# Performance work log

Measured on AMD Instinct MI355X. Metric: run time of the kernel, lower is better.

## Reference

```python
import jax, jax.numpy as jnp
import numpy as np

L = 4096
PI = 3.141592653589793
# cfg weights (V23Config defaults used here)
W_BOND, W_ANGLE, W_RAMA, W_CLASH = 1.0, 1.0, 0.5, 2.0
W_HBOND, W_ELECTRO, W_SOLVENT, W_ROTAMER = 1.0, 0.5, 0.5, 0.5
W_AENT, W_ASMOOTH = 0.01, 0.01
CA_CA_DIST, ANGLE_TARGET_RAD, CLASH_RADIUS = 3.8, 1.5708, 4.0
MOD_BOND, MOD_ANGLE, MOD_CLASH, MOD_HBOND, MOD_RAMA = 0.1, 0.1, 0.1, 0.1, 0.1

# per-residue tables in AA_VOCAB order 'ACDEFGHIKLMNPQRSTVWYX'
CHARGE_TAB = np.zeros(21, np.float32); CHARGE_TAB[[2, 3]] = -1.0; CHARGE_TAB[[8, 14]] = 1.0; CHARGE_TAB[6] = 0.5
HYDRO_TAB = np.array([1.8, 2.5, -3.5, -3.5, 2.8, -0.4, -3.2, 4.5, -3.9, 3.8, 1.9, -3.5, -1.6, -3.5, -4.5, -0.8, -0.7, 4.2, -0.9, -1.3, 0.0], np.float32)
PHI0_TAB = np.full(21, -60.0, np.float32); PHI0_TAB[5] = -75.0; PHI0_TAB[12] = -65.0
PSI0_TAB = np.full(21, -45.0, np.float32); PSI0_TAB[5] = -60.0; PSI0_TAB[12] = -30.0
WID_TAB = np.full(21, 25.0, np.float32); WID_TAB[5] = 40.0; WID_TAB[12] = 20.0
GLY_ID = 5


def _normalize(x, eps=1e-8):
    return x / jnp.maximum(jnp.linalg.norm(x, axis=-1, keepdims=True), eps)


def _cdist(a, b):
    d2 = jnp.sum(a * a, -1)[:, None] + jnp.sum(b * b, -1)[None, :] - 2.0 * (a @ b.T)
    return jnp.sqrt(jnp.maximum(d2, 0.0))


def _dihedral(p0, p1, p2, p3):
    b0, b1, b2 = p1 - p0, p2 - p1, p3 - p2
    b1n = _normalize(b1)
    v = b0 - jnp.sum(b0 * b1n, -1, keepdims=True) * b1n
    w = b2 - jnp.sum(b2 * b1n, -1, keepdims=True) * b1n
    x = jnp.sum(v * w, -1)
    y = jnp.sum(jnp.cross(b1n, v) * w, -1)
    return jnp.arctan2(y + 1e-8, x + 1e-8)


def _energy(ca, alpha, seq_ids):
    Lr = ca.shape[0]
    charge = jnp.asarray(CHARGE_TAB)[seq_ids]
    hydro = jnp.asarray(HYDRO_TAB)[seq_ids]
    phi0 = jnp.asarray(PHI0_TAB)[seq_ids]
    psi0 = jnp.asarray(PSI0_TAB)[seq_ids]
    width = jnp.asarray(WID_TAB)[seq_ids]
    is_gly = seq_ids == GLY_ID

    # ---- reconstruct backbone N, C, O from the CA trace ----
    vn = _normalize(ca[1:] - ca[:-1])  # [L-1,3]
    Natm = jnp.concatenate([ca[:1] - 1.45 * vn[:1], ca[1:] - 1.45 * vn], 0)
    Catm = jnp.concatenate([ca[:-1] + 1.52 * vn, ca[-1:] + 1.52 * vn[-1:]], 0)
    perp = jnp.cross(Catm - ca, Natm - ca)
    pn = jnp.linalg.norm(perp, axis=-1, keepdims=True)
    perp = jnp.where(pn > 1e-6, perp / jnp.maximum(pn, 1e-30), perp)
    Oatm = jnp.concatenate([(Catm + 1.24 * perp)[:-1], Catm[-1:] + jnp.array([0.0, 1.24, 0.0], ca.dtype)], 0)

    # ---- phi/psi dihedrals in degrees ----
    deg = 180.0 / PI
    phi = jnp.zeros(Lr, ca.dtype).at[1:-1].set(_dihedral(Catm[:-2], Natm[1:-1], ca[1:-1], Catm[1:-1])) * deg
    psi = jnp.zeros(Lr, ca.dtype).at[1:-1].set(_dihedral(Natm[1:-1], ca[1:-1], Catm[1:-1], Natm[2:])) * deg

    # ---- bond ----
    target = CA_CA_DIST * (1.0 + MOD_BOND * (alpha - 1.0))
    tpair = 0.5 * (target[1:] + target[:-1])
    d = jnp.linalg.norm(ca[1:] - ca[:-1], axis=-1)
    e_bond = W_BOND * jnp.mean((d - tpair) ** 2)

    # ---- angle ----
    v1 = _normalize(ca[:-2] - ca[1:-1])
    v2 = _normalize(ca[2:] - ca[1:-1])
    cos_ang = jnp.sum(v1 * v2, -1)
    cos_t = jnp.cos(ANGLE_TARGET_RAD * (1.0 + MOD_ANGLE * (alpha[1:-1] - 1.0)))
    e_angle = W_ANGLE * jnp.mean((cos_ang - cos_t) ** 2)

    # ---- rama ----
    weff = width * (1.0 + MOD_RAMA * (alpha - 1.0))
    dphi = (phi - phi0) / (weff + 1e-8)
    dpsi = (psi - psi0) / (weff + 1e-8)
    rmask = jnp.ones(Lr, bool).at[0].set(False).at[-1].set(False)
    e_rama = W_RAMA * jnp.sum((dphi ** 2 + dpsi ** 2) * rmask) / jnp.maximum(1, jnp.sum(rmask))

    D = _cdist(ca, ca)  # [L,L]

    # ---- clash: NOTE the original torch code's advanced indexing
    # mask[idx[:,None], idx[None,:]] = False broadcasts over the FULL grid,
    # so the mask is entirely False and this term is identically zero.
    # Reproduced faithfully (same math).
    radius = CLASH_RADIUS * (1.0 + MOD_CLASH * (alpha[:, None] - 1.0))
    rpair = 0.5 * (radius + radius.T)
    clash = jax.nn.relu(rpair - D) * jnp.zeros((Lr, Lr), ca.dtype)
    e_clash = W_CLASH * jnp.mean(clash ** 2)

    # ---- electrostatics (screened Coulomb) ----
    De = D + 1e-6
    Ee = charge[:, None] * charge[None, :] * jnp.exp(-0.1 * De) / (80.0 * De)
    Ee = Ee * (1.0 - jnp.eye(Lr, dtype=ca.dtype))
    e_electro = W_ELECTRO * jnp.mean(Ee)

    # ---- hydrogen bonds ----
    Dh = _cdist(Oatm, Natm)
    hmask = (Dh > 2.5) & (Dh < 3.5)
    vec_co = (Oatm - Catm)[:, None, :]          # [L,1,3]
    vec_no = Natm[None, :, :] - Oatm[:, None, :]  # [L,L,3]
    num = jnp.sum(vec_co * vec_no, -1)
    den = jnp.maximum(jnp.linalg.norm(vec_co, axis=-1), 1e-8) * jnp.maximum(jnp.linalg.norm(vec_no, axis=-1), 1e-8)
    align = num / den
    ideal = 2.9 * (1.0 + MOD_HBOND * (alpha[:, None] - 1.0))
    Eh = -align * jnp.exp(-(((Dh - ideal) / 0.3) ** 2))
    e_hbond = W_HBOND * jnp.mean(Eh * hmask)

    # ---- solvent / burial ----
    density = jnp.sum((D < 10.0).astype(ca.dtype), -1)
    burial = 1.0 - jnp.exp(-density / 20.0)
    exposed = jnp.where(hydro > 0, hydro * (1.0 - burial), 0.0)
    buried = jnp.where(hydro <= 0, -hydro * burial, 0.0)
    e_solv = W_SOLVENT * jnp.mean(exposed + buried)

    # ---- rotamer (vectorized over residues; skips G and chain ends) ----
    cb_dir = _normalize(-((Natm - ca) + (Catm - ca)))
    ideal_cb = ca + 1.8 * cb_dir
    Dr = _cdist(ideal_cb, ca) + jnp.eye(Lr, dtype=ca.dtype) * 1e9  # exclude self
    dmin = jnp.min(Dr, -1)
    pos = jnp.arange(Lr)
    inc = (~is_gly) & (pos > 0) & (pos < Lr - 1)
    e_rot = W_ROTAMER * jnp.sum(jax.nn.relu(4.0 - dmin) * inc) / max(1, Lr - 2)

    # ---- alpha regularisation ----
    ent = -jnp.mean(alpha * jnp.log(alpha + 1e-8))
    smooth = jnp.mean((alpha[1:] - alpha[:-1]) ** 2)
    e_alpha = W_AENT * ent + W_ASMOOTH * smooth

    return e_bond + e_angle + e_rama + e_clash + e_hbond + e_electro + e_solv + e_rot + e_alpha


def setup_inputs() -> dict:
    key = jax.random.key(0)
    k1, k2, k3 = jax.random.split(key, 3)
    ca = jax.random.normal(k1, (L, 3), jnp.float32) * 10.0  # spread-out CA trace (Angstrom scale)
    alpha = jax.random.uniform(k2, (L,), jnp.float32, 0.5, 3.0)  # AdaptiveAlphaField range
    seq_ids = jax.random.randint(k3, (L,), 0, 21)
    return {"ca": ca, "alpha": alpha, "seq_ids": seq_ids}


def reference(ca, alpha, seq_ids):
    return _energy(ca, alpha, seq_ids)
```

## Files before the change

### kernel.cpp

```cpp
#include <hip/hip_runtime.h>
#include <math.h>

#define L 4096
#define JC 32
#define NJB (L/JC)
#define NIB 8
#define NBLK (NIB*NJB)

__constant__ float c_charge[21] = {0.f,0.f,-1.f,-1.f,0.f,0.f,0.5f,0.f,1.f,0.f,0.f,0.f,0.f,0.f,1.f,0.f,0.f,0.f,0.f,0.f,0.f};
__constant__ float c_hydro[21]  = {1.8f,2.5f,-3.5f,-3.5f,2.8f,-0.4f,-3.2f,4.5f,-3.9f,3.8f,1.9f,-3.5f,-1.6f,-3.5f,-4.5f,-0.8f,-0.7f,4.2f,-0.9f,-1.3f,0.f};
__constant__ float c_phi0[21]   = {-60.f,-60.f,-60.f,-60.f,-60.f,-75.f,-60.f,-60.f,-60.f,-60.f,-60.f,-60.f,-65.f,-60.f,-60.f,-60.f,-60.f,-60.f,-60.f,-60.f,-60.f};
__constant__ float c_psi0[21]   = {-45.f,-45.f,-45.f,-45.f,-45.f,-60.f,-45.f,-45.f,-45.f,-45.f,-45.f,-45.f,-30.f,-45.f,-45.f,-45.f,-45.f,-45.f,-45.f,-45.f,-45.f};
__constant__ float c_wid[21]    = {25.f,25.f,25.f,25.f,25.f,40.f,25.f,25.f,25.f,25.f,25.f,25.f,20.f,25.f,25.f,25.f,25.f,25.f,25.f,25.f,25.f};

#define WS_PA(ws)   ((float4*)(ws))
#define WS_PB(ws)   ((float4*)((ws)+4*L))
#define WS_PI1(ws)  ((float4*)((ws)+8*L))
#define WS_PI2(ws)  ((float4*)((ws)+12*L))
#define WS_PI3(ws)  ((float4*)((ws)+16*L))
#define WS_DENS(ws) ((ws)+20*L)
#define WS_DMIN(ws) ((unsigned int*)((ws)+21*L))
#define WS_RP(ws)   ((ws)+22*L)
#define WS_BPEL(ws) ((ws)+22*L+320)
#define WS_BPHB(ws) ((ws)+22*L+320+NBLK)

struct f3 { float x, y, z; };
__device__ inline f3 mk(float x, float y, float z){ f3 r{x,y,z}; return r; }
__device__ inline f3 sub3(f3 a, f3 b){ return mk(a.x-b.x, a.y-b.y, a.z-b.z); }
__device__ inline f3 add3(f3 a, f3 b){ return mk(a.x+b.x, a.y+b.y, a.z+b.z); }
__device__ inline f3 scl3(f3 a, float s){ return mk(a.x*s, a.y*s, a.z*s); }
__device__ inline float dot3(f3 a, f3 b){ return a.x*b.x + a.y*b.y + a.z*b.z; }
__device__ inline f3 crs3(f3 a, f3 b){ return mk(a.y*b.z-a.z*b.y, a.z*b.x-a.x*b.z, a.x*b.y-a.y*b.x); }
__device__ inline float nrm3(f3 a){ return sqrtf(dot3(a,a)); }
__device__ inline f3 unit3(f3 a){ float n = fmaxf(nrm3(a), 1e-8f); return mk(a.x/n, a.y/n, a.z/n); }

__device__ inline float dihedral(f3 p0, f3 p1, f3 p2, f3 p3){
  f3 b0 = sub3(p1,p0), b1 = sub3(p2,p1), b2 = sub3(p3,p2);
  f3 b1n = unit3(b1);
  f3 v = sub3(b0, scl3(b1n, dot3(b0,b1n)));
  f3 w = sub3(b2, scl3(b1n, dot3(b2,b1n)));
  float x = dot3(v,w);
  float y = dot3(crs3(b1n,v), w);
  return atan2f(y + 1e-8f, x + 1e-8f);
}

__device__ inline float wave_reduce(float v){
  #pragma unroll
  for (int off = 32; off > 0; off >>= 1) v += __shfl_down(v, off, 64);
  return v;
}

__global__ __launch_bounds__(64) void residue_kernel(const float* __restrict__ ca,
    const float* __restrict__ alpha, const int* __restrict__ seq, float* __restrict__ ws)
{
  int i = blockIdx.x*64 + threadIdx.x;
  f3 c0 = mk(ca[3*i], ca[3*i+1], ca[3*i+2]);
  f3 cm = c0, cp = c0;
  if (i > 0)   cm = mk(ca[3*(i-1)], ca[3*(i-1)+1], ca[3*(i-1)+2]);
  if (i < L-1) cp = mk(ca[3*(i+1)], ca[3*(i+1)+1], ca[3*(i+1)+2]);
  f3 vnm = unit3(sub3(c0, cm));
  f3 vni = unit3(sub3(cp, c0));

  f3 N = (i == 0)  ? sub3(c0, scl3(vni, 1.45f)) : sub3(c0, scl3(vnm, 1.45f));
  f3 C = (i < L-1) ? add3(c0, scl3(vni, 1.52f)) : add3(c0, scl3(vnm, 1.52f));
  f3 perp = crs3(sub3(C,c0), sub3(N,c0));
  float pn = nrm3(perp);
  if (pn > 1e-6f) perp = scl3(perp, 1.f/fmaxf(pn, 1e-30f));
  f3 O = (i < L-1) ? add3(C, scl3(perp, 1.24f)) : mk(C.x, C.y + 1.24f, C.z);

  f3 sum = add3(sub3(N,c0), sub3(C,c0));
  f3 cbdir = unit3(mk(-sum.x, -sum.y, -sum.z));
  f3 cb = add3(c0, scl3(cbdir, 1.8f));

  f3 vco = sub3(O, C);
  float nco = fmaxf(nrm3(vco), 1e-8f);

  int sid = seq[i];
  float al = alpha[i];

  float4 pa; pa.x=c0.x; pa.y=c0.y; pa.z=c0.z; pa.w=c_charge[sid];
  float4 pb; pb.x=N.x; pb.y=N.y; pb.z=N.z; pb.w=0.f;
  float4 p1; p1.x=O.x; p1.y=O.y; p1.z=O.z; p1.w=nco;
  float4 p2; p2.x=vco.x; p2.y=vco.y; p2.z=vco.z; p2.w=2.9f*(1.f + 0.1f*(al - 1.f));
  float4 p3; p3.x=cb.x; p3.y=cb.y; p3.z=cb.z; p3.w=0.f;
  WS_PA(ws)[i]=pa; WS_PB(ws)[i]=pb; WS_PI1(ws)[i]=p1; WS_PI2(ws)[i]=p2; WS_PI3(ws)[i]=p3;
  WS_DENS(ws)[i]=0.f;
  WS_DMIN(ws)[i]=0x7F800000u;

  float bond = 0.f, angle = 0.f, rama = 0.f, smooth = 0.f;
  float ent = al * logf(al + 1e-8f);
  if (i < L-1) {
    float alp = alpha[i+1];
    float d = nrm3(sub3(cp, c0));
    float tp = 0.5f*(3.8f*(1.f+0.1f*(al-1.f)) + 3.8f*(1.f+0.1f*(alp-1.f)));
    bond = (d - tp)*(d - tp);
    smooth = (alp - al)*(alp - al);
  }
  if (i >= 1 && i <= L-2) {
    f3 v1 = unit3(sub3(cm, c0));
    f3 v2 = unit3(sub3(cp, c0));
    float cang = dot3(v1, v2);
    float ct = cosf(1.5708f*(1.f + 0.1f*(al - 1.f)));
    angle = (cang - ct)*(cang - ct);

    f3 Cm1 = add3(cm, scl3(vnm, 1.52f));
    f3 Np1 = sub3(cp, scl3(vni, 1.45f));
    const float deg = 57.29577951308232f;
    float phi = dihedral(Cm1, N, c0, C) * deg;
    float psi = dihedral(N, c0, C, Np1) * deg;
    float weff = c_wid[sid]*(1.f + 0.1f*(al - 1.f)) + 1e-8f;
    float dphi = (phi - c_phi0[sid]) / weff;
    float dpsi = (psi - c_psi0[sid]) / weff;
    rama = dphi*dphi + dpsi*dpsi;
  }
  bond = wave_reduce(bond); angle = wave_reduce(angle); rama = wave_reduce(rama);
  ent  = wave_reduce(ent);  smooth = wave_reduce(smooth);
  if (threadIdx.x == 0) {
    float* RP = WS_RP(ws);
    int b = blockIdx.x;
    RP[0*64+b]=bond; RP[1*64+b]=angle; RP[2*64+b]=rama; RP[3*64+b]=ent; RP[4*64+b]=smooth;
  }
}

__global__ __launch_bounds__(256) void pair_kernel(float* __restrict__ ws)
{
  const float4* __restrict__ PA  = WS_PA(ws);
  const float4* __restrict__ PB  = WS_PB(ws);
  const float4* __restrict__ PI1 = WS_PI1(ws);
  const float4* __restrict__ PI2 = WS_PI2(ws);
  const float4* __restrict__ PI3 = WS_PI3(ws);

  int t = threadIdx.x;
  int i0 = blockIdx.x*512 + t;
  int i1 = i0 + 256;
  int j0 = blockIdx.y*JC;

  __shared__ float4 sA[JC];
  __shared__ float4 sB[JC];
  if (t < JC)           sA[t]     = PA[j0 + t];
  else if (t < 2*JC)    sB[t-JC]  = PB[j0 + t - JC];

  float4 a0 = PA[i0],  a1 = PA[i1];
  float4 o0 = PI1[i0], o1 = PI1[i1];
  float4 w0 = PI2[i0], w1 = PI2[i1];
  float4 g0 = PI3[i0], g1 = PI3[i1];
  float rn0 = __builtin_amdgcn_rcpf(o0.w);
  float rn1 = __builtin_amdgcn_rcpf(o1.w);
  __syncthreads();

  float e_el = 0.f, e_hb = 0.f;
  float dens0 = 0.f, dens1 = 0.f, dm0 = 3.0e38f, dm1 = 3.0e38f;

  #pragma unroll 8
  for (int jj = 0; jj < JC; ++jj) {
    float4 a = sA[jj];
    float4 b = sB[jj];
    int jg = j0 + jj;
    bool self0 = (jg == i0), self1 = (jg == i1);

    float dx0 = a0.x - a.x, dy0 = a0.y - a.y, dz0 = a0.z - a.z;
    float d20 = fmaf(dx0,dx0, fmaf(dy0,dy0, dz0*dz0));
    float dx1 = a1.x - a.x, dy1 = a1.y - a.y, dz1 = a1.z - a.z;
    float d21 = fmaf(dx1,dx1, fmaf(dy1,dy1, dz1*dz1));
    dens0 += (d20 < 100.f) ? 1.f : 0.f;
    dens1 += (d21 < 100.f) ? 1.f : 0.f;

    float rx0 = g0.x - a.x, ry0 = g0.y - a.y, rz0 = g0.z - a.z;
    float r20 = fmaf(rx0,rx0, fmaf(ry0,ry0, rz0*rz0));
    dm0 = fminf(dm0, self0 ? 3.0e38f : r20);
    float rx1 = g1.x - a.x, ry1 = g1.y - a.y, rz1 = g1.z - a.z;
    float r21 = fmaf(rx1,rx1, fmaf(ry1,ry1, rz1*rz1));
    dm1 = fminf(dm1, self1 ? 3.0e38f : r21);

    if (a.w != 0.f) {
      float qq0 = self0 ? 0.f : a0.w * a.w;
      float D0  = sqrtf(d20) + 1e-6f;
      e_el += qq0 * __expf(-0.1f*D0) * __builtin_amdgcn_rcpf(80.f*D0);
      float qq1 = self1 ? 0.f : a1.w * a.w;
      float D1  = sqrtf(d21) + 1e-6f;
      e_el += qq1 * __expf(-0.1f*D1) * __builtin_amdgcn_rcpf(80.f*D1);
    }

    float nx0 = b.x - o0.x, ny0 = b.y - o0.y, nz0 = b.z - o0.z;
    float h20 = fmaf(nx0,nx0, fmaf(ny0,ny0, nz0*nz0));
    if (h20 > 6.25f && h20 < 12.25f) {
      float rs  = __builtin_amdgcn_rsqf(h20);
      float Dh  = h20 * rs;
      float num = fmaf(w0.x,nx0, fmaf(w0.y,ny0, w0.z*nz0));
      float tt  = (Dh - w0.w) * 3.33333333333333f;
      e_hb -= num * (rn0 * rs) * __expf(-tt*tt);
    }
    float nx1 = b.x - o1.x, ny1 = b.y - o1.y, nz1 = b.z - o1.z;
    float h21 = fmaf(nx1,nx1, fmaf(ny1,ny1, nz1*nz1));
    if (h21 > 6.25f && h21 < 12.25f) {
      float rs  = __builtin_amdgcn_rsqf(h21);
      float Dh  = h21 * rs;
      float num = fmaf(w1.x,nx1, fmaf(w1.y,ny1, w1.z*nz1));
      float tt  = (Dh - w1.w) * 3.33333333333333f;
      e_hb -= num * (rn1 * rs) * __expf(-tt*tt);
    }
  }

  e_el = wave_reduce(e_el);
  e_hb = wave_reduce(e_hb);
  __shared__ float sp[8];
  if ((t & 63) == 0) { sp[t>>6] = e_el; sp[4+(t>>6)] = e_hb; }
  __syncthreads();
  if (t == 0) {
    int bidx = blockIdx.y*NIB + blockIdx.x;
    WS_BPEL(ws)[bidx] = sp[0]+sp[1]+sp[2]+sp[3];
    WS_BPHB(ws)[bidx] = sp[4]+sp[5]+sp[6]+sp[7];
  }
  atomicAdd(&WS_DENS(ws)[i0], dens0);
  atomicAdd(&WS_DENS(ws)[i1], dens1);
  atomicMin(&WS_DMIN(ws)[i0], __float_as_uint(dm0));
  atomicMin(&WS_DMIN(ws)[i1], __float_as_uint(dm1));
}

__global__ __launch_bounds__(1024) void final_kernel(const int* __restrict__ seq,
    const float* __restrict__ ws, float* __restrict__ out)
{
  int t = threadIdx.x;
  const float* BPel = WS_BPEL(ws);
  const float* BPhb = WS_BPHB(ws);
  const float* RP = WS_RP(ws);

  float v0=0.f,v1=0.f,v2=0.f,v3=0.f,v4=0.f,v7=0.f,v8=0.f;
  float v5 = BPel[t];
  float v6 = BPhb[t];
  if (t < 64) { v0=RP[t]; v1=RP[64+t]; v2=RP[128+t]; v3=RP[192+t]; v4=RP[256+t]; }

  #pragma unroll
  for (int k = 0; k < 4; ++k) {
    int i = t + k*1024;
    float density = WS_DENS((float*)ws)[i];
    float burial = 1.f - __expf(-density * 0.05f);
    float hy = c_hydro[seq[i]];
    v7 += (hy > 0.f) ? hy*(1.f - burial) : (-hy*burial);
    float dmin = sqrtf(__uint_as_float(((const unsigned int*)(ws+21*L))[i]));
    if (seq[i] != 5 && i > 0 && i < L-1) v8 += fmaxf(4.f - dmin, 0.f);
  }

  v0=wave_reduce(v0); v1=wave_reduce(v1); v2=wave_reduce(v2);
  v3=wave_reduce(v3); v4=wave_reduce(v4); v5=wave_reduce(v5);
  v6=wave_reduce(v6); v7=wave_reduce(v7); v8=wave_reduce(v8);

  __shared__ float red[16*9];
  int w = t >> 6;
  if ((t & 63) == 0) {
    red[w*9+0]=v0; red[w*9+1]=v1; red[w*9+2]=v2; red[w*9+3]=v3; red[w*9+4]=v4;
    red[w*9+5]=v5; red[w*9+6]=v6; red[w*9+7]=v7; red[w*9+8]=v8;
  }
  __syncthreads();
  if (t == 0) {
    float s[9];
    #pragma unroll
    for (int q = 0; q < 9; ++q) s[q] = 0.f;
    for (int ww = 0; ww < 16; ++ww)
      #pragma unroll
      for (int q = 0; q < 9; ++q) s[q] += red[ww*9+q];
    const float Lf = (float)L;
    out[0] = s[0] / (Lf - 1.f)
           + s[1] / (Lf - 2.f)
           + 0.5f * s[2] / (Lf - 2.f)
           + 0.5f * s[5] / (Lf * Lf)
           + s[6] / (Lf * Lf)
           + 0.5f * s[7] / Lf
           + 0.5f * s[8] / (Lf - 2.f)
           + 0.01f * (-s[3] / Lf)
           + 0.01f * s[4] / (Lf - 1.f);
  }
}

extern "C" void kernel_launch(void* const* d_in, const int* in_sizes, int n_in,
                              void* d_out, int out_size, void* d_ws, size_t ws_size,
                              hipStream_t stream) {
  (void)in_sizes; (void)n_in; (void)out_size; (void)ws_size;
  const float* ca    = (const float*)d_in[0];
  const float* alpha = (const float*)d_in[1];
  const int*   seq   = (const int*)d_in[2];
  float* out = (float*)d_out;
  float* ws  = (float*)d_ws;

  residue_kernel<<<64, 64, 0, stream>>>(ca, alpha, seq, ws);
  pair_kernel<<<dim3(NIB, NJB), 256, 0, stream>>>(ws);
  final_kernel<<<1, 1024, 0, stream>>>(seq, ws, out);
}
```

Before: 82.49 us.

## Expand pair distances via precomputed norms and halve the j-tile

Squared distances in the pair loop now use the expanded form |a|^2+|b|^2-2a·b. The j-side norms are precomputed in the prep kernel: a new CA-norm array, plus the N norm stored in the spare w lane. The i-side norms and the w·o term are hoisted out of the loop, and the 1/80 electrostatic factor is folded into the charge. The j-tile is halved to 16 with a fully unrolled loop and a launch-bounds occupancy hint, which doubles the number of blocks and the per-element atomics. The final kernel now reads 2048 block partials. The expansion can produce small negative values, so clamps are added before square roots; it also risks cancellation error compared with direct differences.

```diff
diff --git a/kernel.cpp b/kernel.cpp
--- a/kernel.cpp
+++ b/kernel.cpp
@@ -2,7 +2,7 @@
 #include <math.h>
 
 #define L 4096
-#define JC 32
+#define JC 16
 #define NJB (L/JC)
 #define NIB 8
 #define NBLK (NIB*NJB)
@@ -20,9 +20,10 @@
 #define WS_PI3(ws)  ((float4*)((ws)+16*L))
 #define WS_DENS(ws) ((ws)+20*L)
 #define WS_DMIN(ws) ((unsigned int*)((ws)+21*L))
-#define WS_RP(ws)   ((ws)+22*L)
-#define WS_BPEL(ws) ((ws)+22*L+320)
-#define WS_BPHB(ws) ((ws)+22*L+320+NBLK)
+#define WS_CAN(ws)  ((ws)+22*L)
+#define WS_RP(ws)   ((ws)+23*L)
+#define WS_BPEL(ws) ((ws)+23*L+320)
+#define WS_BPHB(ws) ((ws)+23*L+320+NBLK)
 
 struct f3 { float x, y, z; };
 __device__ inline f3 mk(float x, float y, float z){ f3 r{x,y,z}; return r; }
@@ -79,11 +80,12 @@
   float al = alpha[i];
 
   float4 pa; pa.x=c0.x; pa.y=c0.y; pa.z=c0.z; pa.w=c_charge[sid];
-  float4 pb; pb.x=N.x; pb.y=N.y; pb.z=N.z; pb.w=0.f;
+  float4 pb; pb.x=N.x; pb.y=N.y; pb.z=N.z; pb.w=dot3(N,N);
   float4 p1; p1.x=O.x; p1.y=O.y; p1.z=O.z; p1.w=nco;
   float4 p2; p2.x=vco.x; p2.y=vco.y; p2.z=vco.z; p2.w=2.9f*(1.f + 0.1f*(al - 1.f));
   float4 p3; p3.x=cb.x; p3.y=cb.y; p3.z=cb.z; p3.w=0.f;
   WS_PA(ws)[i]=pa; WS_PB(ws)[i]=pb; WS_PI1(ws)[i]=p1; WS_PI2(ws)[i]=p2; WS_PI3(ws)[i]=p3;
+  WS_CAN(ws)[i]=dot3(c0,c0);
   WS_DENS(ws)[i]=0.f;
   WS_DMIN(ws)[i]=0x7F800000u;
 
@@ -122,13 +124,14 @@
   }
 }
 
-__global__ __launch_bounds__(256) void pair_kernel(float* __restrict__ ws)
+__global__ __launch_bounds__(256, 4) void pair_kernel(float* __restrict__ ws)
 {
   const float4* __restrict__ PA  = WS_PA(ws);
   const float4* __restrict__ PB  = WS_PB(ws);
   const float4* __restrict__ PI1 = WS_PI1(ws);
   const float4* __restrict__ PI2 = WS_PI2(ws);
   const float4* __restrict__ PI3 = WS_PI3(ws);
+  const float*  __restrict__ CAN = WS_CAN(ws);
 
   int t = threadIdx.x;
   int i0 = blockIdx.x*512 + t;
@@ -137,13 +140,25 @@
 
   __shared__ float4 sA[JC];
   __shared__ float4 sB[JC];
-  if (t < JC)           sA[t]     = PA[j0 + t];
-  else if (t < 2*JC)    sB[t-JC]  = PB[j0 + t - JC];
+  __shared__ float  sC[JC];
+  if (t < JC)           sA[t]      = PA[j0 + t];
+  else if (t < 2*JC)    sB[t-JC]   = PB[j0 + t - JC];
+  else if (t < 3*JC)    sC[t-2*JC] = CAN[j0 + t - 2*JC];
 
   float4 a0 = PA[i0],  a1 = PA[i1];
   float4 o0 = PI1[i0], o1 = PI1[i1];
   float4 w0 = PI2[i0], w1 = PI2[i1];
   float4 g0 = PI3[i0], g1 = PI3[i1];
+  float a0n = a0.x*a0.x + a0.y*a0.y + a0.z*a0.z;
+  float a1n = a1.x*a1.x + a1.y*a1.y + a1.z*a1.z;
+  float g0n = g0.x*g0.x + g0.y*g0.y + g0.z*g0.z;
+  float g1n = g1.x*g1.x + g1.y*g1.y + g1.z*g1.z;
+  float o0n = o0.x*o0.x + o0.y*o0.y + o0.z*o0.z;
+  float o1n = o1.x*o1.x + o1.y*o1.y + o1.z*o1.z;
+  float wo0 = w0.x*o0.x + w0.y*o0.y + w0.z*o0.z;
+  float wo1 = w1.x*o1.x + w1.y*o1.y + w1.z*o1.z;
+  float q0  = a0.w * 0.0125f;
+  float q1  = a1.w * 0.0125f;
   float rn0 = __builtin_amdgcn_rcpf(o0.w);
   float rn1 = __builtin_amdgcn_rcpf(o1.w);
   __syncthreads();
@@ -151,51 +166,52 @@
   float e_el = 0.f, e_hb = 0.f;
   float dens0 = 0.f, dens1 = 0.f, dm0 = 3.0e38f, dm1 = 3.0e38f;
 
-  #pragma unroll 8
+  #pragma unroll
   for (int jj = 0; jj < JC; ++jj) {
     float4 a = sA[jj];
     float4 b = sB[jj];
+    float canj = sC[jj];
     int jg = j0 + jj;
     bool self0 = (jg == i0), self1 = (jg == i1);
 
-    float dx0 = a0.x - a.x, dy0 = a0.y - a.y, dz0 = a0.z - a.z;
-    float d20 = fmaf(dx0,dx0, fmaf(dy0,dy0, dz0*dz0));
-    float dx1 = a1.x - a.x, dy1 = a1.y - a.y, dz1 = a1.z - a.z;
-    float d21 = fmaf(dx1,dx1, fmaf(dy1,dy1, dz1*dz1));
+    float dca0 = a0.x*a.x + a0.y*a.y + a0.z*a.z;
+    float d20  = fmaf(-2.f, dca0, a0n + canj);
+    float dca1 = a1.x*a.x + a1.y*a.y + a1.z*a.z;
+    float d21  = fmaf(-2.f, dca1, a1n + canj);
     dens0 += (d20 < 100.f) ? 1.f : 0.f;
     dens1 += (d21 < 100.f) ? 1.f : 0.f;
 
-    float rx0 = g0.x - a.x, ry0 = g0.y - a.y, rz0 = g0.z - a.z;
-    float r20 = fmaf(rx0,rx0, fmaf(ry0,ry0, rz0*rz0));
+    float dcb0 = g0.x*a.x + g0.y*a.y + g0.z*a.z;
+    float r20  = fmaf(-2.f, dcb0, g0n + canj);
     dm0 = fminf(dm0, self0 ? 3.0e38f : r20);
-    float rx1 = g1.x - a.x, ry1 = g1.y - a.y, rz1 = g1.z - a.z;
-    float r21 = fmaf(rx1,rx1, fmaf(ry1,ry1, rz1*rz1));
+    float dcb1 = g1.x*a.x + g1.y*a.y + g1.z*a.z;
+    float r21  = fmaf(-2.f, dcb1, g1n + canj);
     dm1 = fminf(dm1, self1 ? 3.0e38f : r21);
 
     if (a.w != 0.f) {
-      float qq0 = self0 ? 0.f : a0.w * a.w;
-      float D0  = sqrtf(d20) + 1e-6f;
-      e_el += qq0 * __expf(-0.1f*D0) * __builtin_amdgcn_rcpf(80.f*D0);
-      float qq1 = self1 ? 0.f : a1.w * a.w;
-      float D1  = sqrtf(d21) + 1e-6f;
-      e_el += qq1 * __expf(-0.1f*D1) * __builtin_amdgcn_rcpf(80.f*D1);
+      float qq0 = self0 ? 0.f : q0 * a.w;
+      float D0  = sqrtf(fmaxf(d20, 0.f)) + 1e-6f;
+      e_el += qq0 * __expf(-0.1f*D0) * __builtin_amdgcn_rcpf(D0);
+      float qq1 = self1 ? 0.f : q1 * a.w;
+      float D1  = sqrtf(fmaxf(d21, 0.f)) + 1e-6f;
+      e_el += qq1 * __expf(-0.1f*D1) * __builtin_amdgcn_rcpf(D1);
     }
 
-    float nx0 = b.x - o0.x, ny0 = b.y - o0.y, nz0 = b.z - o0.z;
-    float h20 = fmaf(nx0,nx0, fmaf(ny0,ny0, nz0*nz0));
+    float don0 = o0.x*b.x + o0.y*b.y + o0.z*b.z;
+    float h20  = fmaf(-2.f, don0, o0n + b.w);
     if (h20 > 6.25f && h20 < 12.25f) {
       float rs  = __builtin_amdgcn_rsqf(h20);
       float Dh  = h20 * rs;
-      float num = fmaf(w0.x,nx0, fmaf(w0.y,ny0, w0.z*nz0));
+      float num = (w0.x*b.x + w0.y*b.y + w0.z*b.z) - wo0;
       float tt  = (Dh - w0.w) * 3.33333333333333f;
       e_hb -= num * (rn0 * rs) * __expf(-tt*tt);
     }
-    float nx1 = b.x - o1.x, ny1 = b.y - o1.y, nz1 = b.z - o1.z;
-    float h21 = fmaf(nx1,nx1, fmaf(ny1,ny1, nz1*nz1));
+    float don1 = o1.x*b.x + o1.y*b.y + o1.z*b.z;
+    float h21  = fmaf(-2.f, don1, o1n + b.w);
     if (h21 > 6.25f && h21 < 12.25f) {
       float rs  = __builtin_amdgcn_rsqf(h21);
       float Dh  = h21 * rs;
-      float num = fmaf(w1.x,nx1, fmaf(w1.y,ny1, w1.z*nz1));
+      float num = (w1.x*b.x + w1.y*b.y + w1.z*b.z) - wo1;
       float tt  = (Dh - w1.w) * 3.33333333333333f;
       e_hb -= num * (rn1 * rs) * __expf(-tt*tt);
     }
@@ -226,8 +242,8 @@
   const float* RP = WS_RP(ws);
 
   float v0=0.f,v1=0.f,v2=0.f,v3=0.f,v4=0.f,v7=0.f,v8=0.f;
-  float v5 = BPel[t];
-  float v6 = BPhb[t];
+  float v5 = BPel[t] + BPel[t+1024];
+  float v6 = BPhb[t] + BPhb[t+1024];
   if (t < 64) { v0=RP[t]; v1=RP[64+t]; v2=RP[128+t]; v3=RP[192+t]; v4=RP[256+t]; }
 
   #pragma unroll
@@ -237,7 +253,7 @@
     float burial = 1.f - __expf(-density * 0.05f);
     float hy = c_hydro[seq[i]];
     v7 += (hy > 0.f) ? hy*(1.f - burial) : (-hy*burial);
-    float dmin = sqrtf(__uint_as_float(((const unsigned int*)(ws+21*L))[i]));
+    float dmin = sqrtf(fmaxf(__uint_as_float(((const unsigned int*)(ws+21*L))[i]), 0.f));
     if (seq[i] != 5 && i > 0 && i < L-1) v8 += fmaxf(4.f - dmin, 0.f);
   }
 
```

Result: slower. 99.85 us (+21.0%).
